# Optimization experiments

Hardware: AMD Instinct MI355X
Metric: run time of the kernel (lower is better)

## Reference

```python
import jax, jax.numpy as jnp
import numpy as np

H, KVH, D, EPS = 8, 4, 64, 1e-5

def _rmsnorm(x, w):
    # normalize over last dim (head_dim)
    norm = jax.lax.rsqrt(jnp.mean(x * x, axis=-1, keepdims=True) + EPS)
    return x * norm * w

def setup_inputs() -> dict:
    key = jax.random.key(0)
    ks = jax.random.split(key, 5)
    B, S, Hid = 2048, 67, 512
    x = jax.random.normal(ks[0], (B, S, Hid), dtype=jnp.float32)
    # weights stored as [in, out] (equivalent to torch Linear weight.T)
    sc = 1.0 / np.sqrt(Hid)
    wq = jax.random.normal(ks[1], (Hid, H * D), dtype=jnp.float32) * sc
    wk = jax.random.normal(ks[2], (Hid, KVH * D), dtype=jnp.float32) * sc
    wv = jax.random.normal(ks[3], (Hid, KVH * D), dtype=jnp.float32) * sc
    wo = jax.random.normal(ks[4], (H * D, Hid), dtype=jnp.float32) * sc
    q_norm_w = jnp.ones((D,), dtype=jnp.float32)
    k_norm_w = jnp.ones((D,), dtype=jnp.float32)
    return {"x": x, "wq": wq, "wk": wk, "wv": wv, "wo": wo,
            "q_norm_w": q_norm_w, "k_norm_w": k_norm_w}

def reference(x, wq, wk, wv, wo, q_norm_w, k_norm_w):
    B, S, _ = x.shape
    G = H // KVH  # query heads per kv head
    q = (x @ wq).reshape(B, S, H, D).transpose(0, 2, 1, 3)      # (B,H,S,D)
    k = (x @ wk).reshape(B, S, KVH, D).transpose(0, 2, 1, 3)    # (B,KVH,S,D)
    v = (x @ wv).reshape(B, S, KVH, D).transpose(0, 2, 1, 3)
    q = _rmsnorm(q, q_norm_w)
    k = _rmsnorm(k, k_norm_w)
    qg = q.reshape(B, KVH, G, S, D)
    scale = 1.0 / np.sqrt(D)
    # bidirectional GQA attention, no mask
    scores = jnp.einsum('bkgsd,bktd->bkgst', qg, k) * scale      # (B,KVH,G,S,S)
    attn = jax.nn.softmax(scores, axis=-1)
    out = jnp.einsum('bkgst,bktd->bkgsd', attn, v)               # (B,KVH,G,S,D)
    out = out.reshape(B, H, S, D).transpose(0, 2, 1, 3).reshape(B, S, H * D)
    return out @ wo
```

## Files before the change

### kernel.cpp

```cpp
#include <hip/hip_runtime.h>
#include <hip/hip_bf16.h>

typedef __attribute__((ext_vector_type(8))) short short8;
typedef __attribute__((ext_vector_type(4))) float f32x4;

#define B_   2048
#define S_   67
#define M_   (B_*S_)
#define HID_ 512
#define H_   8
#define KVH_ 4
#define D_   64

__device__ __forceinline__ unsigned f2bf_u(float f){
  union { __hip_bfloat16 h; unsigned short u; } c; c.h = __float2bfloat16(f); return (unsigned)c.u;
}
__device__ __forceinline__ float bfu2f(unsigned u){
  union { unsigned short u; __hip_bfloat16 h; } c; c.u = (unsigned short)u; return __bfloat162float(c.h);
}
__device__ __forceinline__ unsigned pack2(float a, float b){ return f2bf_u(a) | (f2bf_u(b) << 16); }

__device__ __forceinline__ void unpack8(uint4 v, float* o){
  o[0]=bfu2f(v.x & 0xffffu); o[1]=bfu2f(v.x >> 16);
  o[2]=bfu2f(v.y & 0xffffu); o[3]=bfu2f(v.y >> 16);
  o[4]=bfu2f(v.z & 0xffffu); o[5]=bfu2f(v.z >> 16);
  o[6]=bfu2f(v.w & 0xffffu); o[7]=bfu2f(v.w >> 16);
}

union S8 { short8 v; unsigned short u[8]; };

__global__ __launch_bounds__(256) void cvt_bf16(const float* __restrict__ src,
                                                unsigned short* __restrict__ dst){
  long i = (long)blockIdx.x*256 + threadIdx.x;
  const float4 a = reinterpret_cast<const float4*>(src)[2*i];
  const float4 b = reinterpret_cast<const float4*>(src)[2*i+1];
  uint4 u = { pack2(a.x,a.y), pack2(a.z,a.w), pack2(b.x,b.y), pack2(b.z,b.w) };
  reinterpret_cast<uint4*>(dst)[i] = u;
}

__global__ __launch_bounds__(256) void transpose_w(const float* __restrict__ src, int ncols,
                                                   unsigned short* __restrict__ dst, int row0){
  __shared__ float tile[32][33];
  const int tx = threadIdx.x & 31, ty = threadIdx.x >> 5;
  const int nb = blockIdx.x * 32, kb = blockIdx.y * 32;
  #pragma unroll
  for (int i = 0; i < 4; ++i){
    int r = ty + i*8;
    tile[r][tx] = src[(size_t)(kb + r)*ncols + nb + tx];
  }
  __syncthreads();
  #pragma unroll
  for (int i = 0; i < 4; ++i){
    int r = ty + i*8;
    dst[(size_t)(row0 + nb + r)*512 + kb + tx] = (unsigned short)f2bf_u(tile[tx][r]);
  }
}

template<bool OUT_F32>
__global__ __launch_bounds__(512, 2) void gemm5_k(const unsigned short* __restrict__ A,
                                                  const unsigned short* __restrict__ Bw,
                                                  void* __restrict__ outp, int nbx){
  __shared__ unsigned short Sh[4][2][256*32];

  const int Nld = nbx << 8;
  const int per = gridDim.x >> 3;
  const int wg  = (blockIdx.x & 7) * per + (blockIdx.x >> 3);
  const int m0 = (wg / nbx) * 256;
  const int n0 = (wg % nbx) * 256;

  const int t = threadIdx.x;
  const int l = t & 63;
  const int w = t >> 6;
  const int wr = w >> 2, wc = w & 3;
  const int lr = l & 15, lk = l >> 4;

  const int srow  = w*16 + (l >> 2);
  const int skblk = (l & 3) ^ ((l >> 2) & 3) ^ ((l >> 4) & 3);
  const unsigned short* Ag0 = A  + (size_t)(m0 + srow)*512 + skblk*8;
  const unsigned short* Bg0 = Bw + (size_t)(n0 + srow)*512 + skblk*8;

  const int pk = (lk ^ (lr & 3) ^ ((lr >> 2) & 3)) * 8;

  f32x4 acc[8][4];
  #pragma unroll
  for (int f = 0; f < 8; ++f)
    #pragma unroll
    for (int g = 0; g < 4; ++g) acc[f][g] = (f32x4){0.f, 0.f, 0.f, 0.f};

  short8 bv[4];

#define STAGE_OP_(op_, kt_) do{ \
    const unsigned short* src_ = ((op_) ? Bg0 : Ag0) + (size_t)(kt_)*32; \
    unsigned short* dst_ = &Sh[(kt_)&3][op_][(w*16)*32]; \
    __builtin_amdgcn_global_load_lds((const unsigned int*)src_, (unsigned int*)dst_, 16, 0, 0); \
    __builtin_amdgcn_global_load_lds((const unsigned int*)(src_ + (size_t)128*512), \
                                     (unsigned int*)(dst_ + 128*32), 16, 0, 0); \
  }while(0)

#define PHASE_(kt_, q_) do{ \
    const unsigned short* Asl = &Sh[(kt_)&3][0][0]; \
    const unsigned short* Bsl = &Sh[(kt_)&3][1][0]; \
    short8 av[4]; \
    _Pragma("unroll") \
    for (int f2 = 0; f2 < 4; ++f2) \
      av[f2] = *reinterpret_cast<const short8*>(Asl + (wr*128 + ((q_)*4 + f2)*16 + lr)*32 + pk); \
    if ((q_) == 0){ \
      _Pragma("unroll") \
      for (int g = 0; g < 4; ++g) \
        bv[g] = *reinterpret_cast<const short8*>(Bsl + (wc*64 + g*16 + lr)*32 + pk); \
    } \
    if ((kt_) + 2 <= 15) STAGE_OP_((q_), (kt_) + 2); \
    __builtin_amdgcn_s_barrier(); \
    asm volatile("s_waitcnt lgkmcnt(0)" ::: "memory"); \
    __builtin_amdgcn_sched_barrier(0); \
    __builtin_amdgcn_s_setprio(1); \
    _Pragma("unroll") \
    for (int f2 = 0; f2 < 4; ++f2) \
      _Pragma("unroll") \
      for (int g = 0; g < 4; ++g) \
        acc[(q_)*4 + f2][g] = __builtin_amdgcn_mfma_f32_16x16x32_bf16(av[f2], bv[g], acc[(q_)*4 + f2][g], 0, 0, 0); \
    __builtin_amdgcn_s_setprio(0); \
    if ((q_) == 1){ \
      if ((kt_) < 14)       { asm volatile("s_waitcnt vmcnt(4)" ::: "memory"); } \
      else if ((kt_) == 14) { asm volatile("s_waitcnt vmcnt(0)" ::: "memory"); } \
      __builtin_amdgcn_sched_barrier(0); \
    } \
    __builtin_amdgcn_s_barrier(); \
  }while(0)

  STAGE_OP_(0, 0); STAGE_OP_(1, 0); STAGE_OP_(0, 1); STAGE_OP_(1, 1);
  asm volatile("s_waitcnt vmcnt(4)" ::: "memory");
  __builtin_amdgcn_sched_barrier(0);
  __builtin_amdgcn_s_barrier();

  #pragma unroll
  for (int kt = 0; kt < 16; ++kt){
    PHASE_(kt, 0);
    PHASE_(kt, 1);
  }
#undef PHASE_
#undef STAGE_OP_

  if (OUT_F32){
    float* Cs = reinterpret_cast<float*>(&Sh[0][0][0]);
    float* out = (float*)outp;
    #pragma unroll
    for (int half = 0; half < 2; ++half){
      __syncthreads();
      if (wr == half){
        #pragma unroll
        for (int f = 0; f < 8; ++f)
          #pragma unroll
          for (int g = 0; g < 4; ++g)
            #pragma unroll
            for (int r = 0; r < 4; ++r){
              int row = f*16 + lk*4 + r;
              int col = wc*64 + g*16 + lr;
              Cs[row*256 + col] = acc[f][g][r];
            }
      }
      __syncthreads();
      const float4* Cv = reinterpret_cast<const float4*>(Cs);
      #pragma unroll
      for (int p = 0; p < 16; ++p){
        int idx = p*512 + t;
        int row = idx >> 6, c4 = idx & 63;
        *reinterpret_cast<float4*>(out + (size_t)(m0 + half*128 + row)*Nld + n0 + c4*4) = Cv[idx];
      }
    }
  } else {
    unsigned short* Cs = &Sh[0][0][0];
    unsigned short* out = (unsigned short*)outp;
    #pragma unroll
    for (int half = 0; half < 2; ++half){
      __syncthreads();
      if (wr == half){
        #pragma unroll
        for (int f = 0; f < 8; ++f)
          #pragma unroll
          for (int g = 0; g < 4; ++g)
            #pragma unroll
            for (int r = 0; r < 4; ++r){
              int row = f*16 + lk*4 + r;
              int col = wc*64 + g*16 + lr;
              Cs[row*256 + col] = (unsigned short)f2bf_u(acc[f][g][r]);
            }
      }
      __syncthreads();
      const uint4* Cv = reinterpret_cast<const uint4*>(Cs);
      #pragma unroll
      for (int p = 0; p < 8; ++p){
        int idx = p*512 + t;
        int row = idx >> 5, c16 = idx & 31;
        *reinterpret_cast<uint4*>(out + (size_t)(m0 + half*128 + row)*Nld + n0 + c16*8) = Cv[idx];
      }
    }
  }
}

__global__ __launch_bounds__(576, 5) void attn_k(const unsigned short* __restrict__ qkv,
                                                 const float* __restrict__ qnw,
                                                 const float* __restrict__ knw,
                                                 unsigned short* __restrict__ attn){
  __shared__ unsigned short Vt[64*128];
  __shared__ unsigned short Kf[5][2][64*8];
  __shared__ unsigned short Pb[9][16*128];
  const int t = threadIdx.x;
  const int b = blockIdx.x >> 2, kvh = blockIdx.x & 3;
  const size_t rowbase = (size_t)b * 67;
  const int l = t & 63, w = t >> 6;
  const int lr = l & 15, lk = l >> 4;

  const int vs = t >> 3, vd0 = (t & 7) << 3;
  uint4 vu = {0u,0u,0u,0u};
  if (vs < 67)
    vu = *reinterpret_cast<const uint4*>(qkv + (rowbase + vs)*1024 + 768 + kvh*64 + vd0);
  uint4 ku0 = {0u,0u,0u,0u}, ku1 = {0u,0u,0u,0u};
  if (w < 5){
    int s = w*16 + lr; if (s > 66) s = 66;
    const unsigned short* kp = qkv + (rowbase + s)*1024 + 512 + kvh*64 + lk*8;
    ku0 = *reinterpret_cast<const uint4*>(kp);
    ku1 = *reinterpret_cast<const uint4*>(kp + 32);
  }
  const int qrow = w*16 + lr;
  const int h01 = (qrow >= 67) ? 1 : 0;
  int qr = qrow - (h01 ? 67 : 0); if (qr > 66) qr = 66;
  const unsigned short* qp = qkv + (rowbase + qr)*1024 + (kvh*2 + h01)*64 + lk*8;
  const uint4 qu0 = *reinterpret_cast<const uint4*>(qp);
  const uint4 qu1 = *reinterpret_cast<const uint4*>(qp + 32);
  float wp[16];
  #pragma unroll
  for (int hh = 0; hh < 2; ++hh)
    #pragma unroll
    for (int j = 0; j < 8; ++j){
      int idx = hh*32 + lk*8 + j;
      wp[hh*8+j] = qnw[idx] * knw[idx] * 0.125f;
    }

  {
    unsigned short vsv[8];
    vsv[0]=vu.x&0xffffu; vsv[1]=vu.x>>16; vsv[2]=vu.y&0xffffu; vsv[3]=vu.y>>16;
    vsv[4]=vu.z&0xffffu; vsv[5]=vu.z>>16; vsv[6]=vu.w&0xffffu; vsv[7]=vu.w>>16;
    #pragma unroll
    for (int j = 0; j < 8; ++j){
      int d = vd0 + j;
      int blk = ((vs>>3) ^ (j<<1) ^ (t&7)) & 15;
      Vt[(d<<7) + (blk<<3) + (vs&7)] = vsv[j];
    }
    if (t < 192){
      int s2 = 72 + (t >> 3);
      #pragma unroll
      for (int j = 0; j < 8; ++j){
        int d = vd0 + j;
        int blk = ((s2>>3) ^ (j<<1) ^ (t&7)) & 15;
        Vt[(d<<7) + (blk<<3) + (s2&7)] = 0;
      }
    }
  }

  if (w < 5){
    float f[16]; unpack8(ku0, f); unpack8(ku1, f + 8);
    float ss = 0.f;
    #pragma unroll
    for (int j = 0; j < 16; ++j) ss += f[j]*f[j];
    ss += __shfl_xor(ss, 16); ss += __shfl_xor(ss, 32);
    float inv = rsqrtf(ss*(1.0f/64.0f) + 1e-5f);
    S8 a0, a1;
    #pragma unroll
    for (int j = 0; j < 8; ++j){
      a0.u[j] = (unsigned short)f2bf_u(f[j]   * inv * wp[j]);
      a1.u[j] = (unsigned short)f2bf_u(f[8+j] * inv * wp[8+j]);
    }
    *reinterpret_cast<short8*>(&Kf[w][0][l*8]) = a0.v;
    *reinterpret_cast<short8*>(&Kf[w][1][l*8]) = a1.v;
  }

  short8 qf0, qf1;
  {
    float f[16]; unpack8(qu0, f); unpack8(qu1, f + 8);
    float ss = 0.f;
    #pragma unroll
    for (int j = 0; j < 16; ++j) ss += f[j]*f[j];
    ss += __shfl_xor(ss, 16); ss += __shfl_xor(ss, 32);
    float inv = rsqrtf(ss*(1.0f/64.0f) + 1e-5f);
    S8 a0, a1;
    #pragma unroll
    for (int j = 0; j < 8; ++j){
      a0.u[j] = (unsigned short)f2bf_u(f[j]   * inv);
      a1.u[j] = (unsigned short)f2bf_u(f[8+j] * inv);
    }
    qf0 = a0.v; qf1 = a1.v;
  }

  {
    uint4 z = {0u,0u,0u,0u};
    uint4* pz = reinterpret_cast<uint4*>(Pb[w]);
    #pragma unroll
    for (int i = 0; i < 4; ++i) pz[l + i*64] = z;
  }
  __syncthreads();

  f32x4 sa[5];
  #pragma unroll
  for (int nt = 0; nt < 5; ++nt){
    short8 k0 = *reinterpret_cast<const short8*>(&Kf[nt][0][l*8]);
    short8 k1 = *reinterpret_cast<const short8*>(&Kf[nt][1][l*8]);
    sa[nt] = (f32x4){0.f,0.f,0.f,0.f};
    sa[nt] = __builtin_amdgcn_mfma_f32_16x16x32_bf16(qf0, k0, sa[nt], 0,0,0);
    sa[nt] = __builtin_amdgcn_mfma_f32_16x16x32_bf16(qf1, k1, sa[nt], 0,0,0);
  }

  float inv4[4];
  #pragma unroll
  for (int r = 0; r < 4; ++r){
    float mx = -1e30f;
    #pragma unroll
    for (int nt = 0; nt < 5; ++nt){
      float v = sa[nt][r];
      if (nt*16 + lr >= 67) v = -1e30f;
      sa[nt][r] = v; mx = fmaxf(mx, v);
    }
    mx = fmaxf(mx, __shfl_xor(mx, 1));
    mx = fmaxf(mx, __shfl_xor(mx, 2));
    mx = fmaxf(mx, __shfl_xor(mx, 4));
    mx = fmaxf(mx, __shfl_xor(mx, 8));
    float sm = 0.f;
    #pragma unroll
    for (int nt = 0; nt < 5; ++nt){
      float e = __expf(sa[nt][r] - mx);
      sa[nt][r] = e; sm += e;
    }
    sm += __shfl_xor(sm, 1);
    sm += __shfl_xor(sm, 2);
    sm += __shfl_xor(sm, 4);
    sm += __shfl_xor(sm, 8);
    inv4[r] = 1.0f / sm;
  }

  unsigned short* pb = Pb[w];
  #pragma unroll
  for (int nt = 0; nt < 5; ++nt)
    #pragma unroll
    for (int r = 0; r < 4; ++r){
      int row = lk*4 + r, col = nt*16 + lr;
      int blk = ((col>>3) ^ ((row&7)<<1) ^ (row>>3)) & 15;
      pb[(row<<7) + (blk<<3) + (col&7)] = (unsigned short)f2bf_u(sa[nt][r]);
    }

  f32x4 oa[4];
  #pragma unroll
  for (int dt = 0; dt < 4; ++dt) oa[dt] = (f32x4){0.f,0.f,0.f,0.f};
  #pragma unroll
  for (int ks = 0; ks < 3; ++ks){
    int blkp = ((ks*4 + lk) ^ ((lr&7)<<1) ^ (lr>>3)) & 15;
    short8 pf = *reinterpret_cast<const short8*>(&pb[(lr<<7) + (blkp<<3)]);
    #pragma unroll
    for (int dt = 0; dt < 4; ++dt){
      int d = dt*16 + lr;
      int blkv = ((ks*4 + lk) ^ ((d&7)<<1) ^ (d>>3)) & 15;
      short8 vf = *reinterpret_cast<const short8*>(&Vt[(d<<7) + (blkv<<3)]);
      oa[dt] = __builtin_amdgcn_mfma_f32_16x16x32_bf16(pf, vf, oa[dt], 0,0,0);
    }
  }

  #pragma unroll
  for (int dt = 0; dt < 4; ++dt)
    #pragma unroll
    for (int r = 0; r < 4; ++r){
      int row = w*16 + lk*4 + r;
      if (row < 134){
        int hh = (row >= 67) ? 1 : 0;
        int orow = row - (hh ? 67 : 0);
        attn[(rowbase + orow)*512 + (kvh*2 + hh)*64 + dt*16 + lr] =
            (unsigned short)f2bf_u(oa[dt][r] * inv4[r]);
      }
    }
}

extern "C" void kernel_launch(void* const* d_in, const int* in_sizes, int n_in,
                              void* d_out, int out_size, void* d_ws, size_t ws_size,
                              hipStream_t stream){
  const float* x   = (const float*)d_in[0];
  const float* wq  = (const float*)d_in[1];
  const float* wk  = (const float*)d_in[2];
  const float* wv  = (const float*)d_in[3];
  const float* wo  = (const float*)d_in[4];
  const float* qnw = (const float*)d_in[5];
  const float* knw = (const float*)d_in[6];

  unsigned short* Wt   = (unsigned short*)d_ws;
  unsigned short* Wot  = Wt + 1024*512;
  unsigned short* qkv  = Wot + 512*512;
  unsigned short* attn = qkv + (size_t)M_*1024;
  unsigned short* xb   = attn;

  transpose_w<<<dim3(16,16), 256, 0, stream>>>(wq, 512, Wt, 0);
  transpose_w<<<dim3(8,16),  256, 0, stream>>>(wk, 256, Wt, 512);
  transpose_w<<<dim3(8,16),  256, 0, stream>>>(wv, 256, Wt, 768);
  transpose_w<<<dim3(16,16), 256, 0, stream>>>(wo, 512, Wot, 0);

  cvt_bf16<<<(M_*512/8)/256, 256, 0, stream>>>(x, xb);

  gemm5_k<false><<<dim3(4 * (M_/256)), 512, 0, stream>>>(xb, Wt, qkv, 4);

  attn_k<<<dim3(B_*KVH_), 576, 0, stream>>>(qkv, qnw, knw, attn);

  gemm5_k<true><<<dim3(2 * (M_/256)), 512, 0, stream>>>(attn, Wot, d_out, 2);
}
```

Measured before the change: 580.9 us.

## Process two KV heads per attention block with prefetched loads

Each attention block now handles two (batch, kv-head) items in sequence. All global loads of Q, K and V for both items are issued up front, and the Pb and Vt padding zeroing is done once per block. The goal is to hide global load latency behind the first item's compute and halve block launch overhead. In exchange, register use rises, the launch-bounds occupancy hint drops from 5 to 4, and an extra barrier is added between items.

```diff
diff --git a/kernel.cpp b/kernel.cpp
--- a/kernel.cpp
+++ b/kernel.cpp
@@ -198,7 +198,7 @@
   }
 }
 
-__global__ __launch_bounds__(576, 5) void attn_k(const unsigned short* __restrict__ qkv,
+__global__ __launch_bounds__(576, 4) void attn_k(const unsigned short* __restrict__ qkv,
                                                  const float* __restrict__ qnw,
                                                  const float* __restrict__ knw,
                                                  unsigned short* __restrict__ attn){
@@ -206,28 +206,35 @@
   __shared__ unsigned short Kf[5][2][64*8];
   __shared__ unsigned short Pb[9][16*128];
   const int t = threadIdx.x;
-  const int b = blockIdx.x >> 2, kvh = blockIdx.x & 3;
+  const int item0 = blockIdx.x * 2;
+  const int b = item0 >> 2;
   const size_t rowbase = (size_t)b * 67;
   const int l = t & 63, w = t >> 6;
   const int lr = l & 15, lk = l >> 4;
 
   const int vs = t >> 3, vd0 = (t & 7) << 3;
-  uint4 vu = {0u,0u,0u,0u};
-  if (vs < 67)
-    vu = *reinterpret_cast<const uint4*>(qkv + (rowbase + vs)*1024 + 768 + kvh*64 + vd0);
-  uint4 ku0 = {0u,0u,0u,0u}, ku1 = {0u,0u,0u,0u};
-  if (w < 5){
-    int s = w*16 + lr; if (s > 66) s = 66;
-    const unsigned short* kp = qkv + (rowbase + s)*1024 + 512 + kvh*64 + lk*8;
-    ku0 = *reinterpret_cast<const uint4*>(kp);
-    ku1 = *reinterpret_cast<const uint4*>(kp + 32);
-  }
   const int qrow = w*16 + lr;
   const int h01 = (qrow >= 67) ? 1 : 0;
   int qr = qrow - (h01 ? 67 : 0); if (qr > 66) qr = 66;
-  const unsigned short* qp = qkv + (rowbase + qr)*1024 + (kvh*2 + h01)*64 + lk*8;
-  const uint4 qu0 = *reinterpret_cast<const uint4*>(qp);
-  const uint4 qu1 = *reinterpret_cast<const uint4*>(qp + 32);
+  int ks_ = w*16 + lr; if (ks_ > 66) ks_ = 66;
+
+  uint4 vu[2], ku0[2], ku1[2], qu0[2], qu1[2];
+  #pragma unroll
+  for (int it = 0; it < 2; ++it){
+    const int kvh = (item0 + it) & 3;
+    vu[it] = (uint4){0u,0u,0u,0u};
+    if (vs < 67)
+      vu[it] = *reinterpret_cast<const uint4*>(qkv + (rowbase + vs)*1024 + 768 + kvh*64 + vd0);
+    ku0[it] = (uint4){0u,0u,0u,0u}; ku1[it] = (uint4){0u,0u,0u,0u};
+    if (w < 5){
+      const unsigned short* kp = qkv + (rowbase + ks_)*1024 + 512 + kvh*64 + lk*8;
+      ku0[it] = *reinterpret_cast<const uint4*>(kp);
+      ku1[it] = *reinterpret_cast<const uint4*>(kp + 32);
+    }
+    const unsigned short* qp = qkv + (rowbase + qr)*1024 + (kvh*2 + h01)*64 + lk*8;
+    qu0[it] = *reinterpret_cast<const uint4*>(qp);
+    qu1[it] = *reinterpret_cast<const uint4*>(qp + 32);
+  }
   float wp[16];
   #pragma unroll
   for (int hh = 0; hh < 2; ++hh)
@@ -238,143 +245,150 @@
     }
 
   {
-    unsigned short vsv[8];
-    vsv[0]=vu.x&0xffffu; vsv[1]=vu.x>>16; vsv[2]=vu.y&0xffffu; vsv[3]=vu.y>>16;
-    vsv[4]=vu.z&0xffffu; vsv[5]=vu.z>>16; vsv[6]=vu.w&0xffffu; vsv[7]=vu.w>>16;
+    uint4 z = {0u,0u,0u,0u};
+    uint4* pz = reinterpret_cast<uint4*>(Pb[w]);
+    #pragma unroll
+    for (int i = 0; i < 4; ++i) pz[l + i*64] = z;
+  }
+  if (t < 192){
+    int s2 = 72 + (t >> 3);
     #pragma unroll
     for (int j = 0; j < 8; ++j){
       int d = vd0 + j;
-      int blk = ((vs>>3) ^ (j<<1) ^ (t&7)) & 15;
-      Vt[(d<<7) + (blk<<3) + (vs&7)] = vsv[j];
-    }
-    if (t < 192){
-      int s2 = 72 + (t >> 3);
+      int blk = ((s2>>3) ^ (j<<1) ^ (t&7)) & 15;
+      Vt[(d<<7) + (blk<<3) + (s2&7)] = 0;
+    }
+  }
+
+  #pragma unroll
+  for (int it = 0; it < 2; ++it){
+    const int kvh = (item0 + it) & 3;
+    if (it) __syncthreads();
+
+    {
+      unsigned short vsv[8];
+      uint4 vv = vu[it];
+      vsv[0]=vv.x&0xffffu; vsv[1]=vv.x>>16; vsv[2]=vv.y&0xffffu; vsv[3]=vv.y>>16;
+      vsv[4]=vv.z&0xffffu; vsv[5]=vv.z>>16; vsv[6]=vv.w&0xffffu; vsv[7]=vv.w>>16;
       #pragma unroll
       for (int j = 0; j < 8; ++j){
         int d = vd0 + j;
-        int blk = ((s2>>3) ^ (j<<1) ^ (t&7)) & 15;
-        Vt[(d<<7) + (blk<<3) + (s2&7)] = 0;
-      }
-    }
-  }
-
-  if (w < 5){
-    float f[16]; unpack8(ku0, f); unpack8(ku1, f + 8);
-    float ss = 0.f;
-    #pragma unroll
-    for (int j = 0; j < 16; ++j) ss += f[j]*f[j];
-    ss += __shfl_xor(ss, 16); ss += __shfl_xor(ss, 32);
-    float inv = rsqrtf(ss*(1.0f/64.0f) + 1e-5f);
-    S8 a0, a1;
-    #pragma unroll
-    for (int j = 0; j < 8; ++j){
-      a0.u[j] = (unsigned short)f2bf_u(f[j]   * inv * wp[j]);
-      a1.u[j] = (unsigned short)f2bf_u(f[8+j] * inv * wp[8+j]);
-    }
-    *reinterpret_cast<short8*>(&Kf[w][0][l*8]) = a0.v;
-    *reinterpret_cast<short8*>(&Kf[w][1][l*8]) = a1.v;
-  }
-
-  short8 qf0, qf1;
-  {
-    float f[16]; unpack8(qu0, f); unpack8(qu1, f + 8);
-    float ss = 0.f;
-    #pragma unroll
-    for (int j = 0; j < 16; ++j) ss += f[j]*f[j];
-    ss += __shfl_xor(ss, 16); ss += __shfl_xor(ss, 32);
-    float inv = rsqrtf(ss*(1.0f/64.0f) + 1e-5f);
-    S8 a0, a1;
-    #pragma unroll
-    for (int j = 0; j < 8; ++j){
-      a0.u[j] = (unsigned short)f2bf_u(f[j]   * inv);
-      a1.u[j] = (unsigned short)f2bf_u(f[8+j] * inv);
-    }
-    qf0 = a0.v; qf1 = a1.v;
-  }
-
-  {
-    uint4 z = {0u,0u,0u,0u};
-    uint4* pz = reinterpret_cast<uint4*>(Pb[w]);
-    #pragma unroll
-    for (int i = 0; i < 4; ++i) pz[l + i*64] = z;
-  }
-  __syncthreads();
-
-  f32x4 sa[5];
-  #pragma unroll
-  for (int nt = 0; nt < 5; ++nt){
-    short8 k0 = *reinterpret_cast<const short8*>(&Kf[nt][0][l*8]);
-    short8 k1 = *reinterpret_cast<const short8*>(&Kf[nt][1][l*8]);
-    sa[nt] = (f32x4){0.f,0.f,0.f,0.f};
-    sa[nt] = __builtin_amdgcn_mfma_f32_16x16x32_bf16(qf0, k0, sa[nt], 0,0,0);
-    sa[nt] = __builtin_amdgcn_mfma_f32_16x16x32_bf16(qf1, k1, sa[nt], 0,0,0);
-  }
-
-  float inv4[4];
-  #pragma unroll
-  for (int r = 0; r < 4; ++r){
-    float mx = -1e30f;
+        int blk = ((vs>>3) ^ (j<<1) ^ (t&7)) & 15;
+        if (vs < 72) Vt[(d<<7) + (blk<<3) + (vs&7)] = vsv[j];
+      }
+    }
+
+    if (w < 5){
+      float f[16]; unpack8(ku0[it], f); unpack8(ku1[it], f + 8);
+      float ss = 0.f;
+      #pragma unroll
+      for (int j = 0; j < 16; ++j) ss += f[j]*f[j];
+      ss += __shfl_xor(ss, 16); ss += __shfl_xor(ss, 32);
+      float inv = rsqrtf(ss*(1.0f/64.0f) + 1e-5f);
+      S8 a0, a1;
+      #pragma unroll
+      for (int j = 0; j < 8; ++j){
+        a0.u[j] = (unsigned short)f2bf_u(f[j]   * inv * wp[j]);
+        a1.u[j] = (unsigned short)f2bf_u(f[8+j] * inv * wp[8+j]);
+      }
+      *reinterpret_cast<short8*>(&Kf[w][0][l*8]) = a0.v;
+      *reinterpret_cast<short8*>(&Kf[w][1][l*8]) = a1.v;
+    }
+
+    short8 qf0, qf1;
+    {
+      float f[16]; unpack8(qu0[it], f); unpack8(qu1[it], f + 8);
+      float ss = 0.f;
+      #pragma unroll
+      for (int j = 0; j < 16; ++j) ss += f[j]*f[j];
+      ss += __shfl_xor(ss, 16); ss += __shfl_xor(ss, 32);
+      float inv = rsqrtf(ss*(1.0f/64.0f) + 1e-5f);
+      S8 a0, a1;
+      #pragma unroll
+      for (int j = 0; j < 8; ++j){
+        a0.u[j] = (unsigned short)f2bf_u(f[j]   * inv);
+        a1.u[j] = (unsigned short)f2bf_u(f[8+j] * inv);
+      }
+      qf0 = a0.v; qf1 = a1.v;
+    }
+    __syncthreads();
+
+    f32x4 sa[5];
     #pragma unroll
     for (int nt = 0; nt < 5; ++nt){
-      float v = sa[nt][r];
-      if (nt*16 + lr >= 67) v = -1e30f;
-      sa[nt][r] = v; mx = fmaxf(mx, v);
-    }
-    mx = fmaxf(mx, __shfl_xor(mx, 1));
-    mx = fmaxf(mx, __shfl_xor(mx, 2));
-    mx = fmaxf(mx, __shfl_xor(mx, 4));
-    mx = fmaxf(mx, __shfl_xor(mx, 8));
-    float sm = 0.f;
-    #pragma unroll
-    for (int nt = 0; nt < 5; ++nt){
-      float e = __expf(sa[nt][r] - mx);
-      sa[nt][r] = e; sm += e;
-    }
-    sm += __shfl_xor(sm, 1);
-    sm += __shfl_xor(sm, 2);
-    sm += __shfl_xor(sm, 4);
-    sm += __shfl_xor(sm, 8);
-    inv4[r] = 1.0f / sm;
-  }
-
-  unsigned short* pb = Pb[w];
-  #pragma unroll
-  for (int nt = 0; nt < 5; ++nt)
+      short8 k0 = *reinterpret_cast<const short8*>(&Kf[nt][0][l*8]);
+      short8 k1 = *reinterpret_cast<const short8*>(&Kf[nt][1][l*8]);
+      sa[nt] = (f32x4){0.f,0.f,0.f,0.f};
+      sa[nt] = __builtin_amdgcn_mfma_f32_16x16x32_bf16(qf0, k0, sa[nt], 0,0,0);
+      sa[nt] = __builtin_amdgcn_mfma_f32_16x16x32_bf16(qf1, k1, sa[nt], 0,0,0);
+    }
+
+    float inv4[4];
     #pragma unroll
     for (int r = 0; r < 4; ++r){
-      int row = lk*4 + r, col = nt*16 + lr;
-      int blk = ((col>>3) ^ ((row&7)<<1) ^ (row>>3)) & 15;
-      pb[(row<<7) + (blk<<3) + (col&7)] = (unsigned short)f2bf_u(sa[nt][r]);
-    }
-
-  f32x4 oa[4];
-  #pragma unroll
-  for (int dt = 0; dt < 4; ++dt) oa[dt] = (f32x4){0.f,0.f,0.f,0.f};
-  #pragma unroll
-  for (int ks = 0; ks < 3; ++ks){
-    int blkp = ((ks*4 + lk) ^ ((lr&7)<<1) ^ (lr>>3)) & 15;
-    short8 pf = *reinterpret_cast<const short8*>(&pb[(lr<<7) + (blkp<<3)]);
-    #pragma unroll
-    for (int dt = 0; dt < 4; ++dt){
-      int d = dt*16 + lr;
-      int blkv = ((ks*4 + lk) ^ ((d&7)<<1) ^ (d>>3)) & 15;
-      short8 vf = *reinterpret_cast<const short8*>(&Vt[(d<<7) + (blkv<<3)]);
-      oa[dt] = __builtin_amdgcn_mfma_f32_16x16x32_bf16(pf, vf, oa[dt], 0,0,0);
-    }
-  }
-
-  #pragma unroll
-  for (int dt = 0; dt < 4; ++dt)
-    #pragma unroll
-    for (int r = 0; r < 4; ++r){
-      int row = w*16 + lk*4 + r;
-      if (row < 134){
-        int hh = (row >= 67) ? 1 : 0;
-        int orow = row - (hh ? 67 : 0);
-        attn[(rowbase + orow)*512 + (kvh*2 + hh)*64 + dt*16 + lr] =
-            (unsigned short)f2bf_u(oa[dt][r] * inv4[r]);
-      }
-    }
+      float mx = -1e30f;
+      #pragma unroll
+      for (int nt = 0; nt < 5; ++nt){
+        float v = sa[nt][r];
+        if (nt*16 + lr >= 67) v = -1e30f;
+        sa[nt][r] = v; mx = fmaxf(mx, v);
+      }
+      mx = fmaxf(mx, __shfl_xor(mx, 1));
+      mx = fmaxf(mx, __shfl_xor(mx, 2));
+      mx = fmaxf(mx, __shfl_xor(mx, 4));
+      mx = fmaxf(mx, __shfl_xor(mx, 8));
+      float sm = 0.f;
+      #pragma unroll
+      for (int nt = 0; nt < 5; ++nt){
+        float e = __expf(sa[nt][r] - mx);
+        sa[nt][r] = e; sm += e;
+      }
+      sm += __shfl_xor(sm, 1);
+      sm += __shfl_xor(sm, 2);
+      sm += __shfl_xor(sm, 4);
+      sm += __shfl_xor(sm, 8);
+      inv4[r] = 1.0f / sm;
+    }
+
+    unsigned short* pb = Pb[w];
+    #pragma unroll
+    for (int nt = 0; nt < 5; ++nt)
+      #pragma unroll
+      for (int r = 0; r < 4; ++r){
+        int row = lk*4 + r, col = nt*16 + lr;
+        int blk = ((col>>3) ^ ((row&7)<<1) ^ (row>>3)) & 15;
+        pb[(row<<7) + (blk<<3) + (col&7)] = (unsigned short)f2bf_u(sa[nt][r]);
+      }
+
+    f32x4 oa[4];
+    #pragma unroll
+    for (int dt = 0; dt < 4; ++dt) oa[dt] = (f32x4){0.f,0.f,0.f,0.f};
+    #pragma unroll
+    for (int ks = 0; ks < 3; ++ks){
+      int blkp = ((ks*4 + lk) ^ ((lr&7)<<1) ^ (lr>>3)) & 15;
+      short8 pf = *reinterpret_cast<const short8*>(&pb[(lr<<7) + (blkp<<3)]);
+      #pragma unroll
+      for (int dt = 0; dt < 4; ++dt){
+        int d = dt*16 + lr;
+        int blkv = ((ks*4 + lk) ^ ((d&7)<<1) ^ (d>>3)) & 15;
+        short8 vf = *reinterpret_cast<const short8*>(&Vt[(d<<7) + (blkv<<3)]);
+        oa[dt] = __builtin_amdgcn_mfma_f32_16x16x32_bf16(pf, vf, oa[dt], 0,0,0);
+      }
+    }
+
+    #pragma unroll
+    for (int dt = 0; dt < 4; ++dt)
+      #pragma unroll
+      for (int r = 0; r < 4; ++r){
+        int row = w*16 + lk*4 + r;
+        if (row < 134){
+          int hh = (row >= 67) ? 1 : 0;
+          int orow = row - (hh ? 67 : 0);
+          attn[(rowbase + orow)*512 + (kvh*2 + hh)*64 + dt*16 + lr] =
+              (unsigned short)f2bf_u(oa[dt][r] * inv4[r]);
+        }
+      }
+  }
 }
 
 extern "C" void kernel_launch(void* const* d_in, const int* in_sizes, int n_in,
@@ -403,7 +417,7 @@
 
   gemm5_k<false><<<dim3(4 * (M_/256)), 512, 0, stream>>>(xb, Wt, qkv, 4);
 
-  attn_k<<<dim3(B_*KVH_), 576, 0, stream>>>(qkv, qnw, knw, attn);
+  attn_k<<<dim3(B_*KVH_/2), 576, 0, stream>>>(qkv, qnw, knw, attn);
 
   gemm5_k<true><<<dim3(2 * (M_/256)), 512, 0, stream>>>(attn, Wot, d_out, 2);
 }
```

Result: slower. 598.0 us (+2.9%).

## Fuse fp32-to-bf16 conversion of x into a new QKV projection GEMM

Applied to the files above, without the earlier changes.

Removes the separate cvt_bf16 pass over x and replaces the 256x256 QKV GEMM with a new 128x128-tile kernel that loads fp32 x directly into LDS via global_load_lds and converts to bf16 while building MFMA fragments. This avoids writing and rereading a bf16 copy of the activation. In exchange it reads twice as many bytes of A per tile, converts inside the inner loop, and uses smaller tiles with different occupancy, which could lower MFMA efficiency.

```diff
diff --git a/kernel.cpp b/kernel.cpp
--- a/kernel.cpp
+++ b/kernel.cpp
@@ -29,15 +29,6 @@
 
 union S8 { short8 v; unsigned short u[8]; };
 
-__global__ __launch_bounds__(256) void cvt_bf16(const float* __restrict__ src,
-                                                unsigned short* __restrict__ dst){
-  long i = (long)blockIdx.x*256 + threadIdx.x;
-  const float4 a = reinterpret_cast<const float4*>(src)[2*i];
-  const float4 b = reinterpret_cast<const float4*>(src)[2*i+1];
-  uint4 u = { pack2(a.x,a.y), pack2(a.z,a.w), pack2(b.x,b.y), pack2(b.z,b.w) };
-  reinterpret_cast<uint4*>(dst)[i] = u;
-}
-
 __global__ __launch_bounds__(256) void transpose_w(const float* __restrict__ src, int ncols,
                                                    unsigned short* __restrict__ dst, int row0){
   __shared__ float tile[32][33];
@@ -53,6 +44,114 @@
   for (int i = 0; i < 4; ++i){
     int r = ty + i*8;
     dst[(size_t)(row0 + nb + r)*512 + kb + tx] = (unsigned short)f2bf_u(tile[tx][r]);
+  }
+}
+
+__global__ __launch_bounds__(256, 3) void gemm6_k(const float* __restrict__ A,
+                                                  const unsigned short* __restrict__ Bw,
+                                                  unsigned short* __restrict__ outp, int nbx){
+  __shared__ unsigned short ShA[2][128*64];
+  __shared__ unsigned short ShB[2][128*32];
+
+  const int Nld = nbx << 7;
+  const int per = gridDim.x >> 3;
+  const int wg  = (blockIdx.x & 7) * per + (blockIdx.x >> 3);
+  const int m0 = (wg / nbx) * 128;
+  const int n0 = (wg % nbx) * 128;
+
+  const int t = threadIdx.x;
+  const int l = t & 63;
+  const int w = t >> 6;
+  const int wr = w >> 1, wc = w & 1;
+  const int lr = l & 15, lk = l >> 4;
+
+  const int arow  = w*32 + (l >> 3);
+  const int aslot = (l & 7) ^ (l >> 3);
+  const float* Ag = A + (size_t)(m0 + arow)*512 + aslot*4;
+  const int brow = w*32 + (l >> 2);
+  const int bblk = (l & 3) ^ (brow & 3) ^ ((brow >> 2) & 3);
+  const unsigned short* Bg = Bw + (size_t)(n0 + brow)*512 + bblk*8;
+
+  f32x4 acc[4][4];
+  #pragma unroll
+  for (int f = 0; f < 4; ++f)
+    #pragma unroll
+    for (int g = 0; g < 4; ++g) acc[f][g] = (f32x4){0.f, 0.f, 0.f, 0.f};
+
+#define STAGE6_(tt) do{ \
+    unsigned short* As_ = &ShA[(tt)&1][0]; \
+    unsigned short* Bs_ = &ShB[(tt)&1][0]; \
+    _Pragma("unroll") \
+    for (int j = 0; j < 4; ++j) \
+      __builtin_amdgcn_global_load_lds((const unsigned int*)(Ag + (size_t)(j*8)*512 + (tt)*32), \
+                                       (unsigned int*)(As_ + (w*32 + j*8)*64), 16, 0, 0); \
+    _Pragma("unroll") \
+    for (int j = 0; j < 2; ++j) \
+      __builtin_amdgcn_global_load_lds((const unsigned int*)(Bg + (size_t)(j*16)*512 + (tt)*32), \
+                                       (unsigned int*)(Bs_ + (w*32 + j*16)*32), 16, 0, 0); \
+  }while(0)
+
+  STAGE6_(0);
+  #pragma unroll
+  for (int tt = 0; tt < 16; ++tt){
+    if (tt < 15) STAGE6_(tt + 1);
+    if (tt < 15) asm volatile("s_waitcnt vmcnt(6)" ::: "memory");
+    else         asm volatile("s_waitcnt vmcnt(0)" ::: "memory");
+    __builtin_amdgcn_s_barrier();
+    __builtin_amdgcn_sched_barrier(0);
+
+    const unsigned short* As = &ShA[tt&1][0];
+    const unsigned short* Bs = &ShB[tt&1][0];
+    const int pkb = (lk ^ (lr & 3) ^ ((lr >> 2) & 3)) * 8;
+    const int pa0 = ((lk*2    ) ^ (lr & 7)) * 8;
+    const int pa1 = ((lk*2 + 1) ^ (lr & 7)) * 8;
+    short8 av[4], bv[4];
+    #pragma unroll
+    for (int f = 0; f < 4; ++f){
+      const unsigned short* rb = As + (wr*64 + f*16 + lr)*64;
+      f32x4 lo = *reinterpret_cast<const f32x4*>(rb + pa0);
+      f32x4 hi = *reinterpret_cast<const f32x4*>(rb + pa1);
+      S8 a;
+      #pragma unroll
+      for (int j = 0; j < 4; ++j){
+        a.u[j]   = (unsigned short)f2bf_u(lo[j]);
+        a.u[4+j] = (unsigned short)f2bf_u(hi[j]);
+      }
+      av[f] = a.v;
+      bv[f] = *reinterpret_cast<const short8*>(Bs + (wc*64 + f*16 + lr)*32 + pkb);
+    }
+    __builtin_amdgcn_s_setprio(1);
+    #pragma unroll
+    for (int f = 0; f < 4; ++f)
+      #pragma unroll
+      for (int g = 0; g < 4; ++g)
+        acc[f][g] = __builtin_amdgcn_mfma_f32_16x16x32_bf16(av[f], bv[g], acc[f][g], 0, 0, 0);
+    __builtin_amdgcn_s_setprio(0);
+    asm volatile("s_waitcnt lgkmcnt(0)" ::: "memory");
+    __builtin_amdgcn_sched_barrier(0);
+    __builtin_amdgcn_s_barrier();
+  }
+#undef STAGE6_
+
+  __syncthreads();
+  unsigned short* Cs = &ShA[0][0];
+  #pragma unroll
+  for (int f = 0; f < 4; ++f)
+    #pragma unroll
+    for (int g = 0; g < 4; ++g)
+      #pragma unroll
+      for (int r = 0; r < 4; ++r){
+        int row = wr*64 + f*16 + lk*4 + r;
+        int col = wc*64 + g*16 + lr;
+        Cs[row*128 + col] = (unsigned short)f2bf_u(acc[f][g][r]);
+      }
+  __syncthreads();
+  const uint4* Cv = reinterpret_cast<const uint4*>(Cs);
+  #pragma unroll
+  for (int p = 0; p < 8; ++p){
+    int idx = p*256 + t;
+    int row = idx >> 4, c8 = idx & 15;
+    *reinterpret_cast<uint4*>(outp + (size_t)(m0 + row)*Nld + n0 + c8*8) = Cv[idx];
   }
 }
 
@@ -392,16 +491,13 @@
   unsigned short* Wot  = Wt + 1024*512;
   unsigned short* qkv  = Wot + 512*512;
   unsigned short* attn = qkv + (size_t)M_*1024;
-  unsigned short* xb   = attn;
 
   transpose_w<<<dim3(16,16), 256, 0, stream>>>(wq, 512, Wt, 0);
   transpose_w<<<dim3(8,16),  256, 0, stream>>>(wk, 256, Wt, 512);
   transpose_w<<<dim3(8,16),  256, 0, stream>>>(wv, 256, Wt, 768);
   transpose_w<<<dim3(16,16), 256, 0, stream>>>(wo, 512, Wot, 0);
 
-  cvt_bf16<<<(M_*512/8)/256, 256, 0, stream>>>(x, xb);
-
-  gemm5_k<false><<<dim3(4 * (M_/256)), 512, 0, stream>>>(xb, Wt, qkv, 4);
+  gemm6_k<<<dim3(8 * (M_/128)), 256, 0, stream>>>(x, Wt, qkv, 8);
 
   attn_k<<<dim3(B_*KVH_), 576, 0, stream>>>(qkv, qnw, knw, attn);
 
```

Measured after the change: 599.7 us. 1.03x slower.

## Merge prep kernels into one launch and shrink attention LDS for higher occupancy

Applied to the files above, without the earlier changes.

Combines the four weight-transpose launches and the x-to-bf16 conversion into a single prep kernel, removing four launch gaps. In the attention kernel, the padded V-transpose and probability buffers shrink from 128 to 104 columns with a simpler XOR swizzle, and the launch bound is raised from 5 to 7 blocks per CU, cutting LDS per block to allow more resident blocks. The norm-weight loads move inside the K-normalization branch to reduce register pressure. The new swizzle may introduce LDS bank conflicts, and the tighter register budget may cause spills.

```diff
diff --git a/kernel.cpp b/kernel.cpp
--- a/kernel.cpp
+++ b/kernel.cpp
@@ -29,30 +29,44 @@
 
 union S8 { short8 v; unsigned short u[8]; };
 
-__global__ __launch_bounds__(256) void cvt_bf16(const float* __restrict__ src,
-                                                unsigned short* __restrict__ dst){
-  long i = (long)blockIdx.x*256 + threadIdx.x;
-  const float4 a = reinterpret_cast<const float4*>(src)[2*i];
-  const float4 b = reinterpret_cast<const float4*>(src)[2*i+1];
-  uint4 u = { pack2(a.x,a.y), pack2(a.z,a.w), pack2(b.x,b.y), pack2(b.z,b.w) };
-  reinterpret_cast<uint4*>(dst)[i] = u;
-}
-
-__global__ __launch_bounds__(256) void transpose_w(const float* __restrict__ src, int ncols,
-                                                   unsigned short* __restrict__ dst, int row0){
-  __shared__ float tile[32][33];
-  const int tx = threadIdx.x & 31, ty = threadIdx.x >> 5;
-  const int nb = blockIdx.x * 32, kb = blockIdx.y * 32;
-  #pragma unroll
-  for (int i = 0; i < 4; ++i){
-    int r = ty + i*8;
-    tile[r][tx] = src[(size_t)(kb + r)*ncols + nb + tx];
-  }
-  __syncthreads();
-  #pragma unroll
-  for (int i = 0; i < 4; ++i){
-    int r = ty + i*8;
-    dst[(size_t)(row0 + nb + r)*512 + kb + tx] = (unsigned short)f2bf_u(tile[tx][r]);
+__global__ __launch_bounds__(256) void prep_k(const float* __restrict__ x,
+                                              const float* __restrict__ wq,
+                                              const float* __restrict__ wk,
+                                              const float* __restrict__ wv,
+                                              const float* __restrict__ wo,
+                                              unsigned short* __restrict__ xb,
+                                              unsigned short* __restrict__ Wt,
+                                              unsigned short* __restrict__ Wot){
+  const int blk = blockIdx.x;
+  if (blk < 768){
+    __shared__ float tile[32][33];
+    const float* src; unsigned short* dst; int ncols, row0, nb, kb;
+    if (blk < 256)      { src = wq; dst = Wt;  ncols = 512; row0 = 0;
+                          nb = (blk & 15)*32;        kb = (blk >> 4)*32; }
+    else if (blk < 384) { int g = blk - 256; src = wk; dst = Wt; ncols = 256; row0 = 512;
+                          nb = (g & 7)*32;           kb = (g >> 3)*32; }
+    else if (blk < 512) { int g = blk - 384; src = wv; dst = Wt; ncols = 256; row0 = 768;
+                          nb = (g & 7)*32;           kb = (g >> 3)*32; }
+    else                { int g = blk - 512; src = wo; dst = Wot; ncols = 512; row0 = 0;
+                          nb = (g & 15)*32;          kb = (g >> 4)*32; }
+    const int tx = threadIdx.x & 31, ty = threadIdx.x >> 5;
+    #pragma unroll
+    for (int i = 0; i < 4; ++i){
+      int r = ty + i*8;
+      tile[r][tx] = src[(size_t)(kb + r)*ncols + nb + tx];
+    }
+    __syncthreads();
+    #pragma unroll
+    for (int i = 0; i < 4; ++i){
+      int r = ty + i*8;
+      dst[(size_t)(row0 + nb + r)*512 + kb + tx] = (unsigned short)f2bf_u(tile[tx][r]);
+    }
+  } else {
+    long i = (long)(blk - 768)*256 + threadIdx.x;
+    const float4 a = reinterpret_cast<const float4*>(x)[2*i];
+    const float4 b = reinterpret_cast<const float4*>(x)[2*i+1];
+    uint4 u = { pack2(a.x,a.y), pack2(a.z,a.w), pack2(b.x,b.y), pack2(b.z,b.w) };
+    reinterpret_cast<uint4*>(xb)[i] = u;
   }
 }
 
@@ -198,13 +212,13 @@
   }
 }
 
-__global__ __launch_bounds__(576, 5) void attn_k(const unsigned short* __restrict__ qkv,
+__global__ __launch_bounds__(576, 7) void attn_k(const unsigned short* __restrict__ qkv,
                                                  const float* __restrict__ qnw,
                                                  const float* __restrict__ knw,
                                                  unsigned short* __restrict__ attn){
-  __shared__ unsigned short Vt[64*128];
+  __shared__ unsigned short Vt[64*104];
   __shared__ unsigned short Kf[5][2][64*8];
-  __shared__ unsigned short Pb[9][16*128];
+  __shared__ unsigned short Pb[9][16*104];
   const int t = threadIdx.x;
   const int b = blockIdx.x >> 2, kvh = blockIdx.x & 3;
   const size_t rowbase = (size_t)b * 67;
@@ -228,37 +242,39 @@
   const unsigned short* qp = qkv + (rowbase + qr)*1024 + (kvh*2 + h01)*64 + lk*8;
   const uint4 qu0 = *reinterpret_cast<const uint4*>(qp);
   const uint4 qu1 = *reinterpret_cast<const uint4*>(qp + 32);
-  float wp[16];
-  #pragma unroll
-  for (int hh = 0; hh < 2; ++hh)
-    #pragma unroll
-    for (int j = 0; j < 8; ++j){
-      int idx = hh*32 + lk*8 + j;
-      wp[hh*8+j] = qnw[idx] * knw[idx] * 0.125f;
-    }
 
   {
     unsigned short vsv[8];
     vsv[0]=vu.x&0xffffu; vsv[1]=vu.x>>16; vsv[2]=vu.y&0xffffu; vsv[3]=vu.y>>16;
     vsv[4]=vu.z&0xffffu; vsv[5]=vu.z>>16; vsv[6]=vu.w&0xffffu; vsv[7]=vu.w>>16;
+    const int slot = vs >> 3;
     #pragma unroll
     for (int j = 0; j < 8; ++j){
       int d = vd0 + j;
-      int blk = ((vs>>3) ^ (j<<1) ^ (t&7)) & 15;
-      Vt[(d<<7) + (blk<<3) + (vs&7)] = vsv[j];
+      int phys = slot ^ ((d >> 3) & 3);
+      Vt[d*104 + phys*8 + (vs & 7)] = vsv[j];
     }
     if (t < 192){
       int s2 = 72 + (t >> 3);
+      int slot2 = s2 >> 3;
       #pragma unroll
       for (int j = 0; j < 8; ++j){
         int d = vd0 + j;
-        int blk = ((s2>>3) ^ (j<<1) ^ (t&7)) & 15;
-        Vt[(d<<7) + (blk<<3) + (s2&7)] = 0;
+        int phys = slot2 ^ ((d >> 3) & 3);
+        Vt[d*104 + phys*8 + (s2 & 7)] = 0;
       }
     }
   }
 
   if (w < 5){
+    float wp[16];
+    #pragma unroll
+    for (int hh = 0; hh < 2; ++hh)
+      #pragma unroll
+      for (int j = 0; j < 8; ++j){
+        int idx = hh*32 + lk*8 + j;
+        wp[hh*8+j] = qnw[idx] * knw[idx] * 0.125f;
+      }
     float f[16]; unpack8(ku0, f); unpack8(ku1, f + 8);
     float ss = 0.f;
     #pragma unroll
@@ -295,8 +311,7 @@
   {
     uint4 z = {0u,0u,0u,0u};
     uint4* pz = reinterpret_cast<uint4*>(Pb[w]);
-    #pragma unroll
-    for (int i = 0; i < 4; ++i) pz[l + i*64] = z;
+    for (int i = l; i < 208; i += 64) pz[i] = z;
   }
   __syncthreads();
 
@@ -343,8 +358,8 @@
     #pragma unroll
     for (int r = 0; r < 4; ++r){
       int row = lk*4 + r, col = nt*16 + lr;
-      int blk = ((col>>3) ^ ((row&7)<<1) ^ (row>>3)) & 15;
-      pb[(row<<7) + (blk<<3) + (col&7)] = (unsigned short)f2bf_u(sa[nt][r]);
+      int phys = (col >> 3) ^ ((row >> 3) & 3);
+      pb[row*104 + phys*8 + (col & 7)] = (unsigned short)f2bf_u(sa[nt][r]);
     }
 
   f32x4 oa[4];
@@ -352,13 +367,13 @@
   for (int dt = 0; dt < 4; ++dt) oa[dt] = (f32x4){0.f,0.f,0.f,0.f};
   #pragma unroll
   for (int ks = 0; ks < 3; ++ks){
-    int blkp = ((ks*4 + lk) ^ ((lr&7)<<1) ^ (lr>>3)) & 15;
-    short8 pf = *reinterpret_cast<const short8*>(&pb[(lr<<7) + (blkp<<3)]);
+    int physp = (ks*4 + lk) ^ ((lr >> 3) & 3);
+    short8 pf = *reinterpret_cast<const short8*>(&pb[lr*104 + physp*8]);
     #pragma unroll
     for (int dt = 0; dt < 4; ++dt){
       int d = dt*16 + lr;
-      int blkv = ((ks*4 + lk) ^ ((d&7)<<1) ^ (d>>3)) & 15;
-      short8 vf = *reinterpret_cast<const short8*>(&Vt[(d<<7) + (blkv<<3)]);
+      int physv = (ks*4 + lk) ^ ((d >> 3) & 3);
+      short8 vf = *reinterpret_cast<const short8*>(&Vt[d*104 + physv*8]);
       oa[dt] = __builtin_amdgcn_mfma_f32_16x16x32_bf16(pf, vf, oa[dt], 0,0,0);
     }
   }
@@ -394,12 +409,7 @@
   unsigned short* attn = qkv + (size_t)M_*1024;
   unsigned short* xb   = attn;
 
-  transpose_w<<<dim3(16,16), 256, 0, stream>>>(wq, 512, Wt, 0);
-  transpose_w<<<dim3(8,16),  256, 0, stream>>>(wk, 256, Wt, 512);
-  transpose_w<<<dim3(8,16),  256, 0, stream>>>(wv, 256, Wt, 768);
-  transpose_w<<<dim3(16,16), 256, 0, stream>>>(wo, 512, Wot, 0);
-
-  cvt_bf16<<<(M_*512/8)/256, 256, 0, stream>>>(x, xb);
+  prep_k<<<dim3(768 + M_*512/8/256), 256, 0, stream>>>(x, wq, wk, wv, wo, xb, Wt, Wot);
 
   gemm5_k<false><<<dim3(4 * (M_/256)), 512, 0, stream>>>(xb, Wt, qkv, 4);
 
```

After: 514.5 us, median of 2. -11.4%, faster.
